# Kernel optimization log

Hardware: AMD Instinct MI355X
Metric: run time of the kernel (lower is better)

## Reference

```python
import jax, jax.numpy as jnp
import numpy as np

B, L, D, H = 2, 2048, 1024, 16


def setup_inputs() -> dict:
    key = jax.random.key(0)
    ks = jax.random.split(key, 6)
    return {
        "x": jax.random.normal(ks[0], (B, L, D), dtype=jnp.float32),
        "w_qkv": jax.random.normal(ks[1], (3 * D, D), dtype=jnp.float32) * (D ** -0.5),
        "b_qkv": jax.random.normal(ks[2], (3 * D,), dtype=jnp.float32) * 0.02,
        "w_out": jax.random.normal(ks[3], (D, D), dtype=jnp.float32) * (D ** -0.5),
        "b_out": jax.random.normal(ks[4], (D,), dtype=jnp.float32) * 0.02,
        "lam": jnp.float32(0.5),
        "heads": H,
    }


def reference(x, w_qkv, b_qkv, w_out, b_out, lam, heads):
    b, l, d = x.shape
    dh = d // heads
    scale = d ** -0.5  # NOTE: module scales by d_model**-0.5, not head_dim**-0.5

    qkv = x @ w_qkv.T + b_qkv                      # [B, L, 3D]
    qkv = qkv.reshape(b, l, 3, heads, dh)
    qkv = jnp.transpose(qkv, (2, 0, 3, 1, 4))      # [3, B, H, L, dh]
    q, k, v = qkv[0], qkv[1], qkv[2]

    k_prev = jnp.roll(k, shift=1, axis=2)          # roll along sequence dim

    s_cur = jnp.einsum("bhqd,bhkd->bhqk", q, k) * scale
    s_prev = jnp.einsum("bhqd,bhkd->bhqk", q, k_prev) * scale

    a1 = jax.nn.softmax(s_cur, axis=-1)
    a2 = jax.nn.softmax(s_prev, axis=-1)
    diff = lam * (a1 - a2)                         # dropout = identity (eval)

    o = jnp.einsum("bhqk,bhkd->bhqd", diff, v)     # [B, H, L, dh]
    o = jnp.transpose(o, (0, 2, 1, 3)).reshape(b, l, d)
    return o @ w_out.T + b_out
```

## Files before the change

kernel.cpp:

```cpp
#include <hip/hip_runtime.h>
#include <hip/hip_bf16.h>
#include <stdint.h>


typedef __attribute__((ext_vector_type(8))) short s16x8;
typedef __attribute__((ext_vector_type(4))) float f32x4;

__device__ __forceinline__ float bf2f(unsigned short u) {
    union { unsigned int i; float f; } x; x.i = ((unsigned int)u) << 16; return x.f;
}
__device__ __forceinline__ unsigned short f2bf(float f) {
    union { float f; unsigned int i; } x; x.f = f;
    unsigned int r = x.i + 0x7FFFu + ((x.i >> 16) & 1u);
    return (unsigned short)(r >> 16);
}

__device__ __forceinline__ void gload16(const void* g, void* l) {
    auto gp = reinterpret_cast<const __attribute__((address_space(1))) unsigned int*>(
        reinterpret_cast<uintptr_t>(g));
    auto lp = reinterpret_cast<__attribute__((address_space(3))) unsigned int*>(
        reinterpret_cast<uintptr_t>(l));
    __builtin_amdgcn_global_load_lds(gp, lp, 16, 0, 0);
}

__global__ __launch_bounds__(256) void cvt_all(
    const float* __restrict__ x, const float* __restrict__ wq,
    const float* __restrict__ wo,
    unsigned short* __restrict__ xb, unsigned short* __restrict__ wqb,
    unsigned short* __restrict__ wob)
{
    int i4 = blockIdx.x * 256 + threadIdx.x;
    const float* src; unsigned short* dst; int off;
    if (i4 < 1048576)            { src = x;  dst = xb;  off = i4; }
    else if (i4 < 1048576 + 786432) { src = wq; dst = wqb; off = i4 - 1048576; }
    else                         { src = wo; dst = wob; off = i4 - 1835008; }
    float4 v = ((const float4*)src)[off];
    ushort4 u;
    u.x = f2bf(v.x); u.y = f2bf(v.y); u.z = f2bf(v.z); u.w = f2bf(v.w);
    ((ushort4*)dst)[off] = u;
}

__global__ __launch_bounds__(256) void vd_transpose(
    const unsigned short* __restrict__ qkvb, unsigned short* __restrict__ vdt)
{
    __shared__ unsigned short T[64][72];
    const int tid = threadIdx.x;
    const int j0 = blockIdx.x * 64;
    const int bh = blockIdx.y, b = bh >> 4, h = bh & 15;
    const unsigned short* vb = qkvb + (size_t)b * 2048 * 3072 + 2048 + h * 64;

    int r = tid >> 2, cq = tid & 3;
    int j = j0 + r, jn = (j + 1) & 2047;
    const unsigned short* p0 = vb + (size_t)j  * 3072 + cq * 16;
    const unsigned short* p1 = vb + (size_t)jn * 3072 + cq * 16;
    s16x8 a0 = *(const s16x8*)p0, a1 = *(const s16x8*)(p0 + 8);
    s16x8 b0 = *(const s16x8*)p1, b1 = *(const s16x8*)(p1 + 8);
#pragma unroll
    for (int u = 0; u < 8; ++u)
        T[cq * 16 + u][r] = f2bf(bf2f((unsigned short)a0[u]) - bf2f((unsigned short)b0[u]));
#pragma unroll
    for (int u = 0; u < 8; ++u)
        T[cq * 16 + 8 + u][r] = f2bf(bf2f((unsigned short)a1[u]) - bf2f((unsigned short)b1[u]));
    __syncthreads();

    int row = tid >> 2, sc = tid & 3;
    s16x8 o0 = *(const s16x8*)&T[row][sc * 16];
    s16x8 o1 = *(const s16x8*)&T[row][sc * 16 + 8];
    unsigned short* dst = vdt + ((size_t)bh * 64 + row) * 2048 + j0 + sc * 16;
    *(s16x8*)dst = o0;
    *(s16x8*)(dst + 8) = o1;
}

template <int OUT_BF16>
__global__ __launch_bounds__(256) void gemm_nt_mfma(
    const unsigned short* __restrict__ A,
    const unsigned short* __restrict__ Bm,
    const float* __restrict__ bias,
    void* __restrict__ C,
    int M, int N, int K, int nscale, float smul)
{
    __shared__ unsigned short As[2][128][32];
    __shared__ unsigned short Bs[2][128][32];

    const int tid = threadIdx.x;
    const int wave = tid >> 6, lane = tid & 63;
    const int quad = lane >> 4, ln = lane & 15;
    const int wm = (wave >> 1) * 64, wn = (wave & 1) * 64;
    const int m0 = blockIdx.y * 128, n0 = blockIdx.x * 128;
    const int rA = wave * 16 + (lane >> 2);
    const int gsl = lane & 3;

    f32x4 acc[4][4];
#pragma unroll
    for (int mt = 0; mt < 4; ++mt)
#pragma unroll
        for (int nt = 0; nt < 4; ++nt) acc[mt][nt] = f32x4{0.f, 0.f, 0.f, 0.f};

    auto stage = [&](int p, int k0) {
#pragma unroll
        for (int q = 0; q < 2; ++q) {
            int row = q * 64 + rA;
            int kg = gsl ^ ((row >> 1) & 3);
            gload16(A + (size_t)(m0 + row) * K + k0 + kg * 8,
                    &As[p][q * 64 + wave * 16][0]);
            gload16(Bm + (size_t)(n0 + row) * K + k0 + kg * 8,
                    &Bs[p][q * 64 + wave * 16][0]);
        }
    };

    stage(0, 0);
    __syncthreads();
    int p = 0;
    for (int k0 = 0; k0 < K; k0 += 32) {
        if (k0 + 32 < K) stage(p ^ 1, k0 + 32);
        s16x8 af[4], bfr[4];
#pragma unroll
        for (int mt = 0; mt < 4; ++mt) {
            int rr = wm + mt * 16 + ln;
            af[mt] = *(const s16x8*)&As[p][rr][((quad ^ ((rr >> 1) & 3)) & 3) * 8];
        }
#pragma unroll
        for (int nt = 0; nt < 4; ++nt) {
            int rr = wn + nt * 16 + ln;
            bfr[nt] = *(const s16x8*)&Bs[p][rr][((quad ^ ((rr >> 1) & 3)) & 3) * 8];
        }
#pragma unroll
        for (int mt = 0; mt < 4; ++mt)
#pragma unroll
            for (int nt = 0; nt < 4; ++nt)
                acc[mt][nt] = __builtin_amdgcn_mfma_f32_16x16x32_bf16(
                    af[mt], bfr[nt], acc[mt][nt], 0, 0, 0);
        __syncthreads();
        p ^= 1;
    }

    float bb[4];
#pragma unroll
    for (int nt = 0; nt < 4; ++nt) bb[nt] = bias[n0 + wn + nt * 16 + ln];
#pragma unroll
    for (int mt = 0; mt < 4; ++mt)
#pragma unroll
        for (int nt = 0; nt < 4; ++nt) {
            int col = n0 + wn + nt * 16 + ln;
            float sc = (col < nscale) ? smul : 1.f;
#pragma unroll
            for (int rg = 0; rg < 4; ++rg) {
                int row = m0 + wm + mt * 16 + quad * 4 + rg;
                float v = (acc[mt][nt][rg] + bb[nt]) * sc;
                if (OUT_BF16)
                    ((unsigned short*)C)[(size_t)row * N + col] = f2bf(v);
                else
                    ((float*)C)[(size_t)row * N + col] = v;
            }
        }
}

__global__ __launch_bounds__(256) void diff_attn_v3(
    const unsigned short* __restrict__ qkv,
    const unsigned short* __restrict__ vdt,
    const float* __restrict__ lam_p,
    unsigned short* __restrict__ o_ws)
{
    constexpr int L = 2048, TD = 3072;

    __shared__ unsigned short Ks[2][64][64];
    __shared__ unsigned short Vs[2][64][64];
    __shared__ unsigned short Ps[4][16][64];

    const int tid = threadIdx.x;
    const int wave = tid >> 6, lane = tid & 63;
    const int quad = lane >> 4, ln = lane & 15;
    const int bh = blockIdx.y, b = bh >> 4, h = bh & 15;
    const int q0 = blockIdx.x * 64;
    const size_t seqbase = (size_t)b * L;
    const unsigned short* base = qkv + seqbase * TD + h * 64;
    const unsigned short* kb = base + 1024;
    const unsigned short* vbase = vdt + (size_t)bh * 64 * 2048;

    const int lsl = lane >> 3;
    const int cgl = (lane & 7) ^ lsl;

    s16x8 qf0, qf1;
    {
        const unsigned short* qrow = base + (size_t)(q0 + wave * 16 + ln) * TD;
        qf0 = *(const s16x8*)(qrow + quad * 8);
        qf1 = *(const s16x8*)(qrow + 32 + quad * 8);
    }

    auto stage = [&](int p, int j0) {
        const unsigned short* k0p = kb + (size_t)(j0 + wave * 16 + lsl) * TD + cgl * 8;
        gload16(k0p,                 &Ks[p][wave * 16][0]);
        gload16(k0p + (size_t)8 * TD, &Ks[p][wave * 16 + 8][0]);
        const unsigned short* v0p = vbase + (size_t)(wave * 16 + lsl) * 2048 + j0 + cgl * 8;
        gload16(v0p,            &Vs[p][wave * 16][0]);
        gload16(v0p + 8 * 2048, &Vs[p][wave * 16 + 8][0]);
    };

    f32x4 Oa[4];
    float lsum[4] = {0.f, 0.f, 0.f, 0.f};
#pragma unroll
    for (int t = 0; t < 4; ++t) Oa[t] = f32x4{0.f, 0.f, 0.f, 0.f};

    const int kx0 = (quad ^ (ln & 7)) << 3;
    const int kx1 = ((quad + 4) ^ (ln & 7)) << 3;

    stage(0, 0);
    __syncthreads();
    int p = 0;
    for (int kt = 0; kt < 32; ++kt) {
        if (kt + 1 < 32) stage(p ^ 1, (kt + 1) * 64);

        f32x4 S[4];
#pragma unroll
        for (int t = 0; t < 4; ++t) {
            s16x8 k0 = *(const s16x8*)&Ks[p][t * 16 + ln][kx0];
            s16x8 k1 = *(const s16x8*)&Ks[p][t * 16 + ln][kx1];
            f32x4 z = f32x4{0.f, 0.f, 0.f, 0.f};
            z = __builtin_amdgcn_mfma_f32_16x16x32_bf16(qf0, k0, z, 0, 0, 0);
            z = __builtin_amdgcn_mfma_f32_16x16x32_bf16(qf1, k1, z, 0, 0, 0);
            S[t] = z;
        }

#pragma unroll
        for (int t = 0; t < 4; ++t) {
            int colc = 2 * t + (ln >> 3);
            int wi = ln & 7;
#pragma unroll
            for (int rg = 0; rg < 4; ++rg) {
                float pv = exp2f(S[t][rg]);
                unsigned int bits = __builtin_bit_cast(unsigned int, pv);
                unsigned int tr = bits & 0xFFFF0000u;
                lsum[rg] += __builtin_bit_cast(float, tr);
                int row = quad * 4 + rg;
                Ps[wave][row][((colc ^ (row & 7)) << 3) + wi] =
                    (unsigned short)(bits >> 16);
            }
        }

        s16x8 pf0 = *(const s16x8*)&Ps[wave][ln][kx0];
        s16x8 pf1 = *(const s16x8*)&Ps[wave][ln][kx1];

#pragma unroll
        for (int t = 0; t < 4; ++t) {
            s16x8 v0 = *(const s16x8*)&Vs[p][t * 16 + ln][kx0];
            s16x8 v1 = *(const s16x8*)&Vs[p][t * 16 + ln][kx1];
            Oa[t] = __builtin_amdgcn_mfma_f32_16x16x32_bf16(pf0, v0, Oa[t], 0, 0, 0);
            Oa[t] = __builtin_amdgcn_mfma_f32_16x16x32_bf16(pf1, v1, Oa[t], 0, 0, 0);
        }
        __syncthreads();
        p ^= 1;
    }

    const float lam = lam_p[0];
#pragma unroll
    for (int rg = 0; rg < 4; ++rg) {
        float l = lsum[rg];
        l += __shfl_xor(l, 1);
        l += __shfl_xor(l, 2);
        l += __shfl_xor(l, 4);
        l += __shfl_xor(l, 8);
        float inv = lam / l;
        int row = q0 + wave * 16 + quad * 4 + rg;
#pragma unroll
        for (int t = 0; t < 4; ++t)
            o_ws[(seqbase + row) * 1024 + h * 64 + t * 16 + ln] = f2bf(Oa[t][rg] * inv);
    }
}

extern "C" void kernel_launch(void* const* d_in, const int* in_sizes, int n_in,
                              void* d_out, int out_size, void* d_ws, size_t ws_size,
                              hipStream_t stream) {
    const float* x     = (const float*)d_in[0];
    const float* w_qkv = (const float*)d_in[1];
    const float* b_qkv = (const float*)d_in[2];
    const float* w_out = (const float*)d_in[3];
    const float* b_out = (const float*)d_in[4];
    const float* lam   = (const float*)d_in[5];
    float* out = (float*)d_out;

    unsigned short* xb   = (unsigned short*)d_ws;
    unsigned short* wqb  = xb   + (size_t)4096 * 1024;
    unsigned short* wob  = wqb  + (size_t)3072 * 1024;
    unsigned short* qkvb = wob  + (size_t)1024 * 1024;
    unsigned short* ob   = qkvb + (size_t)4096 * 3072;
    unsigned short* vdt  = ob   + (size_t)4096 * 1024;

    cvt_all<<<8192, 256, 0, stream>>>(x, w_qkv, w_out, xb, wqb, wob);

    gemm_nt_mfma<1><<<dim3(24, 32), 256, 0, stream>>>(
        xb, wqb, b_qkv, qkvb, 4096, 3072, 1024, 1024, 0.045084222f);

    vd_transpose<<<dim3(32, 32), 256, 0, stream>>>(qkvb, vdt);

    diff_attn_v3<<<dim3(32, 32), 256, 0, stream>>>(qkvb, vdt, lam, ob);

    gemm_nt_mfma<0><<<dim3(8, 32), 256, 0, stream>>>(
        ob, wob, b_out, out, 4096, 1024, 1024, 0, 1.f);
}
```

Baseline: 212.4 us.

## Double query rows per attention wave and narrow output GEMM tile

The attention kernel now gives each wave 32 query rows instead of 16. This halves the block count and doubles the reuse of each K/V tile staged into shared memory, at the cost of more accumulator registers per wave. The output projection GEMM gets a templated N tile of 64, which doubles its grid from 256 to 512 blocks for better occupancy across CUs. The exp2 call is also switched to the hardware intrinsic.

```diff
diff --git a/kernel.cpp b/kernel.cpp
--- a/kernel.cpp
+++ b/kernel.cpp
@@ -71,7 +71,7 @@
     *(s16x8*)(dst + 8) = o1;
 }
 
-template <int OUT_BF16>
+template <int OUT_BF16, int BN>
 __global__ __launch_bounds__(256) void gemm_nt_mfma(
     const unsigned short* __restrict__ A,
     const unsigned short* __restrict__ Bm,
@@ -79,22 +79,23 @@
     void* __restrict__ C,
     int M, int N, int K, int nscale, float smul)
 {
+    constexpr int NT = BN / 32;
     __shared__ unsigned short As[2][128][32];
-    __shared__ unsigned short Bs[2][128][32];
+    __shared__ unsigned short Bs[2][BN][32];
 
     const int tid = threadIdx.x;
     const int wave = tid >> 6, lane = tid & 63;
     const int quad = lane >> 4, ln = lane & 15;
-    const int wm = (wave >> 1) * 64, wn = (wave & 1) * 64;
-    const int m0 = blockIdx.y * 128, n0 = blockIdx.x * 128;
+    const int wm = (wave >> 1) * 64, wn = (wave & 1) * (NT * 16);
+    const int m0 = blockIdx.y * 128, n0 = blockIdx.x * BN;
     const int rA = wave * 16 + (lane >> 2);
     const int gsl = lane & 3;
 
-    f32x4 acc[4][4];
+    f32x4 acc[4][NT];
 #pragma unroll
     for (int mt = 0; mt < 4; ++mt)
 #pragma unroll
-        for (int nt = 0; nt < 4; ++nt) acc[mt][nt] = f32x4{0.f, 0.f, 0.f, 0.f};
+        for (int nt = 0; nt < NT; ++nt) acc[mt][nt] = f32x4{0.f, 0.f, 0.f, 0.f};
 
     auto stage = [&](int p, int k0) {
 #pragma unroll
@@ -103,8 +104,9 @@
             int kg = gsl ^ ((row >> 1) & 3);
             gload16(A + (size_t)(m0 + row) * K + k0 + kg * 8,
                     &As[p][q * 64 + wave * 16][0]);
-            gload16(Bm + (size_t)(n0 + row) * K + k0 + kg * 8,
-                    &Bs[p][q * 64 + wave * 16][0]);
+            if (q * 64 < BN)
+                gload16(Bm + (size_t)(n0 + row) * K + k0 + kg * 8,
+                        &Bs[p][q * 64 + wave * 16][0]);
         }
     };
 
@@ -113,34 +115,34 @@
     int p = 0;
     for (int k0 = 0; k0 < K; k0 += 32) {
         if (k0 + 32 < K) stage(p ^ 1, k0 + 32);
-        s16x8 af[4], bfr[4];
+        s16x8 af[4], bfr[NT];
 #pragma unroll
         for (int mt = 0; mt < 4; ++mt) {
             int rr = wm + mt * 16 + ln;
             af[mt] = *(const s16x8*)&As[p][rr][((quad ^ ((rr >> 1) & 3)) & 3) * 8];
         }
 #pragma unroll
-        for (int nt = 0; nt < 4; ++nt) {
+        for (int nt = 0; nt < NT; ++nt) {
             int rr = wn + nt * 16 + ln;
             bfr[nt] = *(const s16x8*)&Bs[p][rr][((quad ^ ((rr >> 1) & 3)) & 3) * 8];
         }
 #pragma unroll
         for (int mt = 0; mt < 4; ++mt)
 #pragma unroll
-            for (int nt = 0; nt < 4; ++nt)
+            for (int nt = 0; nt < NT; ++nt)
                 acc[mt][nt] = __builtin_amdgcn_mfma_f32_16x16x32_bf16(
                     af[mt], bfr[nt], acc[mt][nt], 0, 0, 0);
         __syncthreads();
         p ^= 1;
     }
 
-    float bb[4];
-#pragma unroll
-    for (int nt = 0; nt < 4; ++nt) bb[nt] = bias[n0 + wn + nt * 16 + ln];
+    float bb[NT];
+#pragma unroll
+    for (int nt = 0; nt < NT; ++nt) bb[nt] = bias[n0 + wn + nt * 16 + ln];
 #pragma unroll
     for (int mt = 0; mt < 4; ++mt)
 #pragma unroll
-        for (int nt = 0; nt < 4; ++nt) {
+        for (int nt = 0; nt < NT; ++nt) {
             int col = n0 + wn + nt * 16 + ln;
             float sc = (col < nscale) ? smul : 1.f;
 #pragma unroll
@@ -155,7 +157,7 @@
         }
 }
 
-__global__ __launch_bounds__(256) void diff_attn_v3(
+__global__ __launch_bounds__(256) void diff_attn_v4(
     const unsigned short* __restrict__ qkv,
     const unsigned short* __restrict__ vdt,
     const float* __restrict__ lam_p,
@@ -165,13 +167,13 @@
 
     __shared__ unsigned short Ks[2][64][64];
     __shared__ unsigned short Vs[2][64][64];
-    __shared__ unsigned short Ps[4][16][64];
+    __shared__ unsigned short Ps[4][32][64];
 
     const int tid = threadIdx.x;
     const int wave = tid >> 6, lane = tid & 63;
     const int quad = lane >> 4, ln = lane & 15;
     const int bh = blockIdx.y, b = bh >> 4, h = bh & 15;
-    const int q0 = blockIdx.x * 64;
+    const int q0 = blockIdx.x * 128;
     const size_t seqbase = (size_t)b * L;
     const unsigned short* base = qkv + seqbase * TD + h * 64;
     const unsigned short* kb = base + 1024;
@@ -180,26 +182,34 @@
     const int lsl = lane >> 3;
     const int cgl = (lane & 7) ^ lsl;
 
-    s16x8 qf0, qf1;
-    {
-        const unsigned short* qrow = base + (size_t)(q0 + wave * 16 + ln) * TD;
-        qf0 = *(const s16x8*)(qrow + quad * 8);
-        qf1 = *(const s16x8*)(qrow + 32 + quad * 8);
+    s16x8 qf[2][2];
+#pragma unroll
+    for (int s = 0; s < 2; ++s) {
+        const unsigned short* qrow =
+            base + (size_t)(q0 + wave * 32 + s * 16 + ln) * TD;
+        qf[s][0] = *(const s16x8*)(qrow + quad * 8);
+        qf[s][1] = *(const s16x8*)(qrow + 32 + quad * 8);
     }
 
     auto stage = [&](int p, int j0) {
         const unsigned short* k0p = kb + (size_t)(j0 + wave * 16 + lsl) * TD + cgl * 8;
-        gload16(k0p,                 &Ks[p][wave * 16][0]);
+        gload16(k0p,                  &Ks[p][wave * 16][0]);
         gload16(k0p + (size_t)8 * TD, &Ks[p][wave * 16 + 8][0]);
         const unsigned short* v0p = vbase + (size_t)(wave * 16 + lsl) * 2048 + j0 + cgl * 8;
         gload16(v0p,            &Vs[p][wave * 16][0]);
         gload16(v0p + 8 * 2048, &Vs[p][wave * 16 + 8][0]);
     };
 
-    f32x4 Oa[4];
-    float lsum[4] = {0.f, 0.f, 0.f, 0.f};
-#pragma unroll
-    for (int t = 0; t < 4; ++t) Oa[t] = f32x4{0.f, 0.f, 0.f, 0.f};
+    f32x4 Oa[2][4];
+    float lsum[2][4];
+#pragma unroll
+    for (int s = 0; s < 2; ++s)
+#pragma unroll
+        for (int t = 0; t < 4; ++t) Oa[s][t] = f32x4{0.f, 0.f, 0.f, 0.f};
+#pragma unroll
+    for (int s = 0; s < 2; ++s)
+#pragma unroll
+        for (int rg = 0; rg < 4; ++rg) lsum[s][rg] = 0.f;
 
     const int kx0 = (quad ^ (ln & 7)) << 3;
     const int kx1 = ((quad + 4) ^ (ln & 7)) << 3;
@@ -210,42 +220,54 @@
     for (int kt = 0; kt < 32; ++kt) {
         if (kt + 1 < 32) stage(p ^ 1, (kt + 1) * 64);
 
-        f32x4 S[4];
+        f32x4 S[2][4];
 #pragma unroll
         for (int t = 0; t < 4; ++t) {
             s16x8 k0 = *(const s16x8*)&Ks[p][t * 16 + ln][kx0];
             s16x8 k1 = *(const s16x8*)&Ks[p][t * 16 + ln][kx1];
-            f32x4 z = f32x4{0.f, 0.f, 0.f, 0.f};
-            z = __builtin_amdgcn_mfma_f32_16x16x32_bf16(qf0, k0, z, 0, 0, 0);
-            z = __builtin_amdgcn_mfma_f32_16x16x32_bf16(qf1, k1, z, 0, 0, 0);
-            S[t] = z;
-        }
-
-#pragma unroll
-        for (int t = 0; t < 4; ++t) {
-            int colc = 2 * t + (ln >> 3);
-            int wi = ln & 7;
-#pragma unroll
-            for (int rg = 0; rg < 4; ++rg) {
-                float pv = exp2f(S[t][rg]);
-                unsigned int bits = __builtin_bit_cast(unsigned int, pv);
-                unsigned int tr = bits & 0xFFFF0000u;
-                lsum[rg] += __builtin_bit_cast(float, tr);
-                int row = quad * 4 + rg;
-                Ps[wave][row][((colc ^ (row & 7)) << 3) + wi] =
-                    (unsigned short)(bits >> 16);
+#pragma unroll
+            for (int s = 0; s < 2; ++s) {
+                f32x4 z = f32x4{0.f, 0.f, 0.f, 0.f};
+                z = __builtin_amdgcn_mfma_f32_16x16x32_bf16(qf[s][0], k0, z, 0, 0, 0);
+                z = __builtin_amdgcn_mfma_f32_16x16x32_bf16(qf[s][1], k1, z, 0, 0, 0);
+                S[s][t] = z;
             }
         }
 
-        s16x8 pf0 = *(const s16x8*)&Ps[wave][ln][kx0];
-        s16x8 pf1 = *(const s16x8*)&Ps[wave][ln][kx1];
+#pragma unroll
+        for (int s = 0; s < 2; ++s)
+#pragma unroll
+            for (int t = 0; t < 4; ++t) {
+                int colc = 2 * t + (ln >> 3);
+                int wi = ln & 7;
+#pragma unroll
+                for (int rg = 0; rg < 4; ++rg) {
+                    float pv = __builtin_amdgcn_exp2f(S[s][t][rg]);
+                    unsigned int bits = __builtin_bit_cast(unsigned int, pv);
+                    unsigned int tr = bits & 0xFFFF0000u;
+                    lsum[s][rg] += __builtin_bit_cast(float, tr);
+                    int row = quad * 4 + rg;
+                    Ps[wave][s * 16 + row][((colc ^ (row & 7)) << 3) + wi] =
+                        (unsigned short)(bits >> 16);
+                }
+            }
+
+        s16x8 pf[2][2];
+#pragma unroll
+        for (int s = 0; s < 2; ++s) {
+            pf[s][0] = *(const s16x8*)&Ps[wave][s * 16 + ln][kx0];
+            pf[s][1] = *(const s16x8*)&Ps[wave][s * 16 + ln][kx1];
+        }
 
 #pragma unroll
         for (int t = 0; t < 4; ++t) {
             s16x8 v0 = *(const s16x8*)&Vs[p][t * 16 + ln][kx0];
             s16x8 v1 = *(const s16x8*)&Vs[p][t * 16 + ln][kx1];
-            Oa[t] = __builtin_amdgcn_mfma_f32_16x16x32_bf16(pf0, v0, Oa[t], 0, 0, 0);
-            Oa[t] = __builtin_amdgcn_mfma_f32_16x16x32_bf16(pf1, v1, Oa[t], 0, 0, 0);
+#pragma unroll
+            for (int s = 0; s < 2; ++s) {
+                Oa[s][t] = __builtin_amdgcn_mfma_f32_16x16x32_bf16(pf[s][0], v0, Oa[s][t], 0, 0, 0);
+                Oa[s][t] = __builtin_amdgcn_mfma_f32_16x16x32_bf16(pf[s][1], v1, Oa[s][t], 0, 0, 0);
+            }
         }
         __syncthreads();
         p ^= 1;
@@ -253,18 +275,21 @@
 
     const float lam = lam_p[0];
 #pragma unroll
-    for (int rg = 0; rg < 4; ++rg) {
-        float l = lsum[rg];
-        l += __shfl_xor(l, 1);
-        l += __shfl_xor(l, 2);
-        l += __shfl_xor(l, 4);
-        l += __shfl_xor(l, 8);
-        float inv = lam / l;
-        int row = q0 + wave * 16 + quad * 4 + rg;
-#pragma unroll
-        for (int t = 0; t < 4; ++t)
-            o_ws[(seqbase + row) * 1024 + h * 64 + t * 16 + ln] = f2bf(Oa[t][rg] * inv);
-    }
+    for (int s = 0; s < 2; ++s)
+#pragma unroll
+        for (int rg = 0; rg < 4; ++rg) {
+            float l = lsum[s][rg];
+            l += __shfl_xor(l, 1);
+            l += __shfl_xor(l, 2);
+            l += __shfl_xor(l, 4);
+            l += __shfl_xor(l, 8);
+            float inv = lam / l;
+            int row = q0 + wave * 32 + s * 16 + quad * 4 + rg;
+#pragma unroll
+            for (int t = 0; t < 4; ++t)
+                o_ws[(seqbase + row) * 1024 + h * 64 + t * 16 + ln] =
+                    f2bf(Oa[s][t][rg] * inv);
+        }
 }
 
 extern "C" void kernel_launch(void* const* d_in, const int* in_sizes, int n_in,
@@ -287,13 +312,13 @@
 
     cvt_all<<<8192, 256, 0, stream>>>(x, w_qkv, w_out, xb, wqb, wob);
 
-    gemm_nt_mfma<1><<<dim3(24, 32), 256, 0, stream>>>(
+    gemm_nt_mfma<1, 128><<<dim3(24, 32), 256, 0, stream>>>(
         xb, wqb, b_qkv, qkvb, 4096, 3072, 1024, 1024, 0.045084222f);
 
     vd_transpose<<<dim3(32, 32), 256, 0, stream>>>(qkvb, vdt);
 
-    diff_attn_v3<<<dim3(32, 32), 256, 0, stream>>>(qkvb, vdt, lam, ob);
-
-    gemm_nt_mfma<0><<<dim3(8, 32), 256, 0, stream>>>(
+    diff_attn_v4<<<dim3(16, 32), 256, 0, stream>>>(qkvb, vdt, lam, ob);
+
+    gemm_nt_mfma<0, 64><<<dim3(16, 32), 256, 0, stream>>>(
         ob, wob, b_out, out, 4096, 1024, 1024, 0, 1.f);
 }
```

Result: faster. 202.9 us (-4.5%).
